# Kernel optimization log

Measured on AMD Instinct MI355X. Metric: run time of the kernel, lower is better.

Reference implementation:

```python
import jax, jax.numpy as jnp
import numpy as np

N_HEAD = 16
MASK_SCALE = 10000.0  # matches torch buffer construction


def setup_inputs() -> dict:
    key = jax.random.key(0)
    k1, k2 = jax.random.split(key)
    B, T, C = 2, 2048, 1024
    x = jax.random.normal(k1, (B, T, C), dtype=jnp.float32)
    # packed q,k projection: nn.Linear(C, 2C, bias=False) -> weight [2C, C]
    W_attn = jax.random.normal(k2, (2 * C, C), dtype=jnp.float32) * 0.02
    alpha = jnp.array(1.0, dtype=jnp.float32)
    beta = jnp.array(0.1, dtype=jnp.float32)
    gamma = jnp.array(0.1, dtype=jnp.float32)
    return {"x": x, "W_attn": W_attn, "alpha": alpha, "beta": beta, "gamma": gamma}


def _shaped_attention(x, W_attn, alpha, beta, gamma):
    B, T, C = x.shape
    H = N_HEAD
    hd = C // H
    # packed projection then split into q, k (use_v=False -> v comes from x)
    qk = jnp.einsum('btc,oc->bto', x, W_attn)  # [B,T,2C]
    q, k = jnp.split(qk, 2, axis=-1)
    q = q.reshape(B, T, H, hd).transpose(0, 2, 1, 3)  # [B,H,T,hd]
    k = k.reshape(B, T, H, hd).transpose(0, 2, 1, 3)
    v = x.reshape(B, T, H, hd).transpose(0, 2, 1, 3)

    scores = jnp.einsum('bhqd,bhkd->bhqk', q, k) * (hd ** -0.5)
    tril = jnp.tril(jnp.ones((T, T), dtype=bool))
    scores = jnp.where(tril, scores, -jnp.inf)
    att = jax.nn.softmax(scores, axis=-1)  # [B,H,T,T]

    # fixed structured masks, built exactly as the torch buffers
    Id = jax.nn.softmax(jnp.eye(T, dtype=jnp.float32) * MASK_SCALE, axis=-1)
    MC = jax.nn.softmax(tril.astype(jnp.float32) * MASK_SCALE, axis=-1)

    shaped = beta * att + alpha * Id[None, None] - gamma * MC[None, None]
    y = jnp.einsum('bhqk,bhkd->bhqd', shaped, v)
    return y.transpose(0, 2, 1, 3).reshape(B, T, C)  # c_proj is Identity


def reference(x, W_attn, alpha, beta, gamma):
    return _shaped_attention(x, W_attn, alpha, beta, gamma)
```

## Files before the change

### kernel.cpp

```cpp
#include <hip/hip_runtime.h>
#include <hip/hip_bf16.h>

typedef __attribute__((ext_vector_type(8))) short bf16x8;
typedef __attribute__((ext_vector_type(4))) float f32x4;
typedef unsigned short u16;

#define B_  2
#define T_  2048
#define C_  1024
#define H_  16
#define HD_ 64

static __device__ __forceinline__ u16 f2bf(float f) {
  unsigned u = __float_as_uint(f);
  u += 0x7fffu + ((u >> 16) & 1u);
  return (u16)(u >> 16);
}

#define NW4 524288
__global__ __launch_bounds__(256) void prep(
    const float* __restrict__ X, const float* __restrict__ W,
    u16* __restrict__ Xb, u16* __restrict__ Wb,
    u16* __restrict__ Vf, float* __restrict__ SubP64)
{
  __shared__ u16 tr[64][65];
  __shared__ float cs[4][64];
  const int blk = blockIdx.x;
  const int tid = threadIdx.x;

  if (blk < 1024) {
    const int kt = blk & 31, bh = blk >> 5;
    const int b = bh >> 4, h = bh & 15;
    const int w = tid >> 6, lane = tid & 63;
    {
      const int row = tid >> 2;
      const int c0  = (tid & 3) * 16;
      const float* xp = X + ((size_t)b * T_ + kt * 64 + row) * C_ + h * 64 + c0;
      float vals[16];
#pragma unroll
      for (int q = 0; q < 4; ++q) {
        float4 v = *(const float4*)(xp + q * 4);
        vals[q * 4 + 0] = v.x; vals[q * 4 + 1] = v.y;
        vals[q * 4 + 2] = v.z; vals[q * 4 + 3] = v.w;
      }
      u16 xb[16];
#pragma unroll
      for (int i = 0; i < 16; ++i) xb[i] = f2bf(vals[i]);
      u16* xq = Xb + ((size_t)(b * T_ + kt * 64 + row)) * C_ + h * 64 + c0;
      *(bf16x8*)xq       = *(const bf16x8*)&xb[0];
      *(bf16x8*)(xq + 8) = *(const bf16x8*)&xb[8];
#pragma unroll
      for (int i = 0; i < 16; ++i) tr[row][c0 + i] = xb[i];
#pragma unroll
      for (int m = 4; m <= 32; m <<= 1)
#pragma unroll
        for (int i = 0; i < 16; ++i) vals[i] += __shfl_xor(vals[i], m);
      if (lane < 4) {
        float* dst = &cs[w][lane * 16];
#pragma unroll
        for (int q = 0; q < 4; ++q) {
          f32x4 s4 = { vals[q * 4 + 0], vals[q * 4 + 1], vals[q * 4 + 2], vals[q * 4 + 3] };
          *(f32x4*)&dst[q * 4] = s4;
        }
      }
    }
    __syncthreads();
    {
      const int quad = (lane >> 4), l16 = lane & 15;
      u16* outb = Vf + ((size_t)bh * 32 + kt) * 4096;
#pragma unroll
      for (int c = 0; c < 2; ++c) {
        u16 tmp[8];
#pragma unroll
        for (int j = 0; j < 8; ++j) tmp[j] = tr[c * 32 + quad * 8 + j][w * 16 + l16];
        *(bf16x8*)&outb[((w * 2 + c) * 64 + lane) * 8] = *(const bf16x8*)tmp;
      }
    }
    if (tid < 64)
      SubP64[(size_t)bh * 2048 + kt * 64 + tid] =
          cs[0][tid] + cs[1][tid] + cs[2][tid] + cs[3][tid];
  } else {
    int i = (blk - 1024) * 256 + tid;
    float4 v = ((const float4*)W)[i];
    ushort4 u = { f2bf(v.x), f2bf(v.y), f2bf(v.z), f2bf(v.w) };
    ((ushort4*)Wb)[i] = u;
  }
}

__global__ __launch_bounds__(256) void gemm_qk(
    const u16* __restrict__ Xb, const u16* __restrict__ Wb,
    u16* __restrict__ Qo, u16* __restrict__ Kf)
{
  __shared__ __align__(16) u16 As[2][128 * 64];
  __shared__ __align__(16) u16 Bs[2][128 * 64];

  const int tid  = threadIdx.x;
  const int w    = tid >> 6;
  const int lane = tid & 63;
  const int quad = lane >> 4;
  const int l16  = lane & 15;
  const int m0 = blockIdx.y * 128;
  const int n0 = blockIdx.x * 128;

  const int grow = w * 8 + ((lane >> 3) & 7);
  const int gcol = (lane & 7) * 8;

  f32x4 zero = {0.f, 0.f, 0.f, 0.f};
  f32x4 acc[4][4];
#pragma unroll
  for (int i = 0; i < 4; ++i)
#pragma unroll
    for (int j = 0; j < 4; ++j) acc[i][j] = zero;

  const int wr = (w >> 1) * 64, wc = (w & 1) * 64;

  const u16* gax = Xb + (size_t)(m0 + grow) * C_ + gcol;
  const u16* gbx = Wb + (size_t)(n0 + grow) * C_ + gcol;

#define GISSUE(K, BUF)                                                      \
  {                                                                         \
    _Pragma("unroll") for (int r = 0; r < 4; ++r) {                         \
      __builtin_amdgcn_global_load_lds(                                     \
          (const __attribute__((address_space(1))) void*)(gax + (size_t)r * 32 * C_ + (K)), \
          (__attribute__((address_space(3))) void*)&As[BUF][(w * 8 + r * 32) * 64], \
          16, 0, 0);                                                        \
      __builtin_amdgcn_global_load_lds(                                     \
          (const __attribute__((address_space(1))) void*)(gbx + (size_t)r * 32 * C_ + (K)), \
          (__attribute__((address_space(3))) void*)&Bs[BUF][(w * 8 + r * 32) * 64], \
          16, 0, 0);                                                        \
    }                                                                       \
  }

  GISSUE(0, 0);
#pragma unroll 2
  for (int it = 0; it < 16; ++it) {
    const int cur = it & 1;
    __syncthreads();
    if (it < 15) GISSUE((it + 1) * 64, cur ^ 1);
#pragma unroll
    for (int c = 0; c < 2; ++c) {
      bf16x8 af[4], bf[4];
#pragma unroll
      for (int i = 0; i < 4; ++i)
        af[i] = *(const bf16x8*)&As[cur][(wr + i * 16 + l16) * 64 + c * 32 + quad * 8];
#pragma unroll
      for (int j = 0; j < 4; ++j)
        bf[j] = *(const bf16x8*)&Bs[cur][(wc + j * 16 + l16) * 64 + c * 32 + quad * 8];
#pragma unroll
      for (int i = 0; i < 4; ++i)
#pragma unroll
        for (int j = 0; j < 4; ++j)
          acc[i][j] = __builtin_amdgcn_mfma_f32_16x16x32_bf16(af[i], bf[j], acc[i][j], 0, 0, 0);
    }
  }
#undef GISSUE

#pragma unroll
  for (int i = 0; i < 4; ++i) {
    const int t_base = m0 + wr + i * 16;
    const int bidx = t_base >> 11;
    const int kt   = (t_base & 2047) >> 6;
    const int trow = (t_base & 2047) + quad * 4;
#pragma unroll
    for (int j = 0; j < 4; ++j) {
      const int n = n0 + wc + j * 16 + l16;
      if (n < C_) {
        const int hq = n >> 6, d = n & 63;
        u16* qp = Qo + (((size_t)bidx * H_ + hq) * T_ + trow) * HD_ + d;
#pragma unroll
        for (int r = 0; r < 4; ++r) qp[(size_t)r * HD_] = f2bf(0.125f * acc[i][j][r]);
      } else {
        const int nh = n - C_;
        const int hh = nh >> 6, d = nh & 63;
        u16* kp = Kf + (((((size_t)(bidx * H_ + hh) * 32 + kt) * 4 + i) * 2 + (d >> 5)) * 64
                        + ((d >> 3) & 3) * 16 + quad * 4) * 8 + (d & 7);
#pragma unroll
        for (int r = 0; r < 4; ++r) kp[(size_t)r * 8] = f2bf(acc[i][j][r]);
      }
    }
  }
}

__device__ __forceinline__ void load_kv(
    bf16x8 (&kf)[2][4], bf16x8 (&vf)[2][4],
    const u16* __restrict__ kbase, const u16* __restrict__ vbase, int lane)
{
#pragma unroll
  for (int c = 0; c < 2; ++c)
#pragma unroll
    for (int nb = 0; nb < 4; ++nb) {
      kf[c][nb] = *(const bf16x8*)&kbase[((nb * 2 + c) * 64 + lane) * 8];
      vf[c][nb] = *(const bf16x8*)&vbase[((nb * 2 + c) * 64 + lane) * 8];
    }
}

__device__ __forceinline__ void tile_compute(
    const bf16x8 (&qfrag)[2], const bf16x8 (&kf)[2][4], const bf16x8 (&vf)[2][4],
    f32x4 (&acc)[4], f32x4& accl, float (*pb)[68],
    int quad, int l16, int myrow, bool diag, bf16x8 onesf)
{
  f32x4 zero = {0.f, 0.f, 0.f, 0.f};
  f32x4 sfr[4] = {zero, zero, zero, zero};
#pragma unroll
  for (int cc = 0; cc < 2; ++cc)
#pragma unroll
    for (int nb = 0; nb < 4; ++nb)
      sfr[nb] = __builtin_amdgcn_mfma_f32_16x16x32_bf16(qfrag[cc], kf[cc][nb], sfr[nb], 0, 0, 0);

#pragma unroll
  for (int nb = 0; nb < 4; ++nb)
#pragma unroll
    for (int r = 0; r < 4; ++r) {
      float p = __expf(sfr[nb][r]);
      if (diag && (nb * 16 + l16 > myrow + r)) p = 0.f;
      pb[quad * 4 + r][nb * 16 + l16] = p;
    }

#pragma unroll
  for (int cc = 0; cc < 2; ++cc) {
    f32x4 plo = *(const f32x4*)&pb[l16][cc * 32 + quad * 8];
    f32x4 phi = *(const f32x4*)&pb[l16][cc * 32 + quad * 8 + 4];
    union { unsigned u[4]; bf16x8 v; } pk;
    __hip_bfloat162 hh;
    hh = __float22bfloat162_rn(make_float2(plo[0], plo[1])); pk.u[0] = *(unsigned*)&hh;
    hh = __float22bfloat162_rn(make_float2(plo[2], plo[3])); pk.u[1] = *(unsigned*)&hh;
    hh = __float22bfloat162_rn(make_float2(phi[0], phi[1])); pk.u[2] = *(unsigned*)&hh;
    hh = __float22bfloat162_rn(make_float2(phi[2], phi[3])); pk.u[3] = *(unsigned*)&hh;
    accl = __builtin_amdgcn_mfma_f32_16x16x32_bf16(pk.v, onesf, accl, 0, 0, 0);
#pragma unroll
    for (int nb = 0; nb < 4; ++nb)
      acc[nb] = __builtin_amdgcn_mfma_f32_16x16x32_bf16(pk.v, vf[cc][nb], acc[nb], 0, 0, 0);
  }
}

__global__ __launch_bounds__(256) void attn_kernel(
    const u16* __restrict__ Q, const u16* __restrict__ Kf, const u16* __restrict__ Vf,
    const float* __restrict__ SubP64, const float* __restrict__ X, float* __restrict__ out,
    const float* __restrict__ alphap, const float* __restrict__ betap,
    const float* __restrict__ gammap)
{
  __shared__ __align__(16) char smem[19456];

  const int tid  = threadIdx.x;
  const int w    = tid >> 6;
  const int lane = tid & 63;
  const int quad = lane >> 4;
  const int l16  = lane & 15;
  const int qt = 31 - blockIdx.y;
  const int bh = blockIdx.x;
  const int b = bh >> 4, h = bh & 15;

  const u16* kfb = Kf + (size_t)bh * T_ * HD_;
  const u16* vfb = Vf + (size_t)bh * T_ * HD_;

  bf16x8 qfrag[2];
  {
    const u16* qp = Q + ((size_t)bh * T_ + qt * 64 + w * 16 + l16) * HD_ + quad * 8;
    qfrag[0] = *(const bf16x8*)qp;
    qfrag[1] = *(const bf16x8*)(qp + 32);
  }

  bf16x8 onesf;
#pragma unroll
  for (int j = 0; j < 8; ++j) onesf[j] = (short)0x3F80;

  f32x4 zero = {0.f, 0.f, 0.f, 0.f};
  f32x4 acc[4] = {zero, zero, zero, zero};
  f32x4 accl = zero;
  const int myrow = w * 16 + quad * 4;
  float (*pb)[68] = (float(*)[68])((float*)smem + (size_t)w * 16 * 68);

  bf16x8 kA[2][4], vA[2][4], kB[2][4], vB[2][4];
  load_kv(kA, vA, kfb, vfb, lane);
  int kt = 0;
  for (;;) {
    int ktn = (kt + 1 < qt) ? kt + 1 : qt;
    load_kv(kB, vB, kfb + (size_t)ktn * 4096, vfb + (size_t)ktn * 4096, lane);
    tile_compute(qfrag, kA, vA, acc, accl, pb, quad, l16, myrow, kt == qt, onesf);
    if (kt + 1 > qt) break;
    int ktn2 = (kt + 2 < qt) ? kt + 2 : qt;
    load_kv(kA, vA, kfb + (size_t)ktn2 * 4096, vfb + (size_t)ktn2 * 4096, lane);
    tile_compute(qfrag, kB, vB, acc, accl, pb, quad, l16, myrow, kt + 1 == qt, onesf);
    kt += 2;
    if (kt > qt) break;
  }

  __syncthreads();
  float* Xt = (float*)smem;
  float* G  = (float*)(smem + 17408);
  float* GP = (float*)(smem + 18432);

  {
    const int row = tid >> 2, c0 = (tid & 3) * 16;
    const float* xp = X + ((size_t)b * T_ + qt * 64 + row) * C_ + h * 64 + c0;
#pragma unroll
    for (int q = 0; q < 4; ++q) {
      float4 v = *(const float4*)(xp + q * 4);
      Xt[row * 68 + c0 + q * 4 + 0] = v.x;
      Xt[row * 68 + c0 + q * 4 + 1] = v.y;
      Xt[row * 68 + c0 + q * 4 + 2] = v.z;
      Xt[row * 68 + c0 + q * 4 + 3] = v.w;
    }
  }
  {
    float p = 0.f;
    for (int i = w; i < qt; i += 4)
      p += SubP64[(size_t)bh * 2048 + i * 64 + lane];
    GP[w * 64 + lane] = p;
  }
  __syncthreads();
  {
    float g = 0.f;
#pragma unroll
    for (int i = 0; i < 16; ++i) g += Xt[(w * 16 + i) * 68 + lane];
    G[w * 64 + lane] = g;
  }
  __syncthreads();
  {
    const float alpha = *alphap, gamma = *gammap;
    float run = GP[lane] + GP[64 + lane] + GP[128 + lane] + GP[192 + lane];
    for (int g = 0; g < w; ++g) run += G[g * 64 + lane];
    const int tbase = qt * 64 + w * 16;
#pragma unroll
    for (int i = 0; i < 16; ++i) {
      float v = Xt[(w * 16 + i) * 68 + lane];
      run += v;
      Xt[(w * 16 + i) * 68 + lane] =
          alpha * v - gamma * run * __builtin_amdgcn_rcpf((float)(tbase + i + 1));
    }
  }
  __syncthreads();

  const float beta = *betap;
  float rl[4];
#pragma unroll
  for (int r = 0; r < 4; ++r) rl[r] = beta * __builtin_amdgcn_rcpf(accl[r]);
#pragma unroll
  for (int nb = 0; nb < 4; ++nb) {
#pragma unroll
    for (int r = 0; r < 4; ++r) {
      int t = qt * 64 + myrow + r;
      int d = nb * 16 + l16;
      out[((size_t)b * T_ + t) * C_ + h * 64 + d] =
          Xt[(myrow + r) * 68 + d] + rl[r] * acc[nb][r];
    }
  }
}

extern "C" void kernel_launch(void* const* d_in, const int* in_sizes, int n_in,
                              void* d_out, int out_size, void* d_ws, size_t ws_size,
                              hipStream_t stream) {
  const float* x      = (const float*)d_in[0];
  const float* W_attn = (const float*)d_in[1];
  const float* alphap = (const float*)d_in[2];
  const float* betap  = (const float*)d_in[3];
  const float* gammap = (const float*)d_in[4];
  float* out = (float*)d_out;

  char* ws = (char*)d_ws;
  u16*   Qb     = (u16*)(ws);
  u16*   Kfb    = (u16*)(ws + (8ull  << 20));
  u16*   Vfb    = (u16*)(ws + (16ull << 20));
  float* SubP64 = (float*)(ws + (24ull << 20));
  u16*   Xb     = (u16*)(ws + (25ull << 20));
  u16*   Wb     = (u16*)(ws + (33ull << 20));

  prep<<<3072, 256, 0, stream>>>(x, W_attn, Xb, Wb, Vfb, SubP64);
  gemm_qk<<<dim3(16, 32), 256, 0, stream>>>(Xb, Wb, Qb, Kfb);
  attn_kernel<<<dim3(32, 32), 256, 0, stream>>>(Qb, Kfb, Vfb, SubP64, x, out,
                                                alphap, betap, gammap);
}
```

Before: 151.1 us.

## Split attention key loop across two wave groups per block and combine partials

Result: slower. 310.7 us (+105.7%).

```diff
diff --git a/kernel.cpp b/kernel.cpp
--- a/kernel.cpp
+++ b/kernel.cpp
@@ -66,6 +66,7 @@
     }
     __syncthreads();
     {
+      const int w = tid >> 6, lane = tid & 63;
       const int quad = (lane >> 4), l16 = lane & 15;
       u16* outb = Vf + ((size_t)bh * 32 + kt) * 4096;
 #pragma unroll
@@ -233,16 +234,18 @@
   }
 }
 
-__global__ __launch_bounds__(256) void attn_kernel(
+__global__ __launch_bounds__(512, 6) void attn_kernel(
     const u16* __restrict__ Q, const u16* __restrict__ Kf, const u16* __restrict__ Vf,
     const float* __restrict__ SubP64, const float* __restrict__ X, float* __restrict__ out,
     const float* __restrict__ alphap, const float* __restrict__ betap,
     const float* __restrict__ gammap)
 {
-  __shared__ __align__(16) char smem[19456];
+  __shared__ __align__(16) char smem[34816];
 
   const int tid  = threadIdx.x;
   const int w    = tid >> 6;
+  const int wq   = w & 3;
+  const int half = w >> 2;
   const int lane = tid & 63;
   const int quad = lane >> 4;
   const int l16  = lane & 15;
@@ -255,7 +258,7 @@
 
   bf16x8 qfrag[2];
   {
-    const u16* qp = Q + ((size_t)bh * T_ + qt * 64 + w * 16 + l16) * HD_ + quad * 8;
+    const u16* qp = Q + ((size_t)bh * T_ + qt * 64 + wq * 16 + l16) * HD_ + quad * 8;
     qfrag[0] = *(const bf16x8*)qp;
     qfrag[1] = *(const bf16x8*)(qp + 32);
   }
@@ -267,34 +270,57 @@
   f32x4 zero = {0.f, 0.f, 0.f, 0.f};
   f32x4 acc[4] = {zero, zero, zero, zero};
   f32x4 accl = zero;
-  const int myrow = w * 16 + quad * 4;
+  const int myrow = wq * 16 + quad * 4;
   float (*pb)[68] = (float(*)[68])((float*)smem + (size_t)w * 16 * 68);
 
-  bf16x8 kA[2][4], vA[2][4], kB[2][4], vB[2][4];
-  load_kv(kA, vA, kfb, vfb, lane);
-  int kt = 0;
-  for (;;) {
-    int ktn = (kt + 1 < qt) ? kt + 1 : qt;
-    load_kv(kB, vB, kfb + (size_t)ktn * 4096, vfb + (size_t)ktn * 4096, lane);
-    tile_compute(qfrag, kA, vA, acc, accl, pb, quad, l16, myrow, kt == qt, onesf);
-    if (kt + 1 > qt) break;
-    int ktn2 = (kt + 2 < qt) ? kt + 2 : qt;
-    load_kv(kA, vA, kfb + (size_t)ktn2 * 4096, vfb + (size_t)ktn2 * 4096, lane);
-    tile_compute(qfrag, kB, vB, acc, accl, pb, quad, l16, myrow, kt + 1 == qt, onesf);
-    kt += 2;
-    if (kt > qt) break;
+  if (half <= qt) {
+    bf16x8 kA[2][4], vA[2][4], kB[2][4], vB[2][4];
+    int kt = half;
+    load_kv(kA, vA, kfb + (size_t)kt * 4096, vfb + (size_t)kt * 4096, lane);
+    for (;;) {
+      int ktn = (kt + 2 <= qt) ? kt + 2 : kt;
+      load_kv(kB, vB, kfb + (size_t)ktn * 4096, vfb + (size_t)ktn * 4096, lane);
+      tile_compute(qfrag, kA, vA, acc, accl, pb, quad, l16, myrow, kt == qt, onesf);
+      if (kt + 2 > qt) break;
+      int ktn2 = (kt + 4 <= qt) ? kt + 4 : kt + 2;
+      load_kv(kA, vA, kfb + (size_t)ktn2 * 4096, vfb + (size_t)ktn2 * 4096, lane);
+      tile_compute(qfrag, kB, vB, acc, accl, pb, quad, l16, myrow, kt + 2 == qt, onesf);
+      kt += 4;
+      if (kt > qt) break;
+    }
   }
 
   __syncthreads();
+  {
+    float* comb = (float*)smem;
+    if (half == 1) {
+      float* dst = comb + ((size_t)(wq * 64 + lane)) * 20;
+#pragma unroll
+      for (int nb = 0; nb < 4; ++nb) *(f32x4*)&dst[nb * 4] = acc[nb];
+      *(f32x4*)&dst[16] = accl;
+    }
+    __syncthreads();
+    if (half == 0) {
+      const float* src = comb + ((size_t)(wq * 64 + lane)) * 20;
+#pragma unroll
+      for (int nb = 0; nb < 4; ++nb) {
+        f32x4 t = *(const f32x4*)&src[nb * 4];
+        acc[nb] += t;
+      }
+      accl += *(const f32x4*)&src[16];
+    }
+  }
+  __syncthreads();
+
   float* Xt = (float*)smem;
   float* G  = (float*)(smem + 17408);
-  float* GP = (float*)(smem + 18432);
-
-  {
-    const int row = tid >> 2, c0 = (tid & 3) * 16;
+  float* GP = (float*)(smem + 19456);
+
+  {
+    const int row = tid >> 3, c0 = (tid & 7) * 8;
     const float* xp = X + ((size_t)b * T_ + qt * 64 + row) * C_ + h * 64 + c0;
 #pragma unroll
-    for (int q = 0; q < 4; ++q) {
+    for (int q = 0; q < 2; ++q) {
       float4 v = *(const float4*)(xp + q * 4);
       Xt[row * 68 + c0 + q * 4 + 0] = v.x;
       Xt[row * 68 + c0 + q * 4 + 1] = v.y;
@@ -304,7 +330,7 @@
   }
   {
     float p = 0.f;
-    for (int i = w; i < qt; i += 4)
+    for (int i = w; i < qt; i += 8)
       p += SubP64[(size_t)bh * 2048 + i * 64 + lane];
     GP[w * 64 + lane] = p;
   }
@@ -312,37 +338,41 @@
   {
     float g = 0.f;
 #pragma unroll
-    for (int i = 0; i < 16; ++i) g += Xt[(w * 16 + i) * 68 + lane];
+    for (int i = 0; i < 8; ++i) g += Xt[(w * 8 + i) * 68 + lane];
     G[w * 64 + lane] = g;
   }
   __syncthreads();
   {
     const float alpha = *alphap, gamma = *gammap;
-    float run = GP[lane] + GP[64 + lane] + GP[128 + lane] + GP[192 + lane];
+    float run = 0.f;
+#pragma unroll
+    for (int k = 0; k < 8; ++k) run += GP[k * 64 + lane];
     for (int g = 0; g < w; ++g) run += G[g * 64 + lane];
-    const int tbase = qt * 64 + w * 16;
-#pragma unroll
-    for (int i = 0; i < 16; ++i) {
-      float v = Xt[(w * 16 + i) * 68 + lane];
+    const int tbase = qt * 64 + w * 8;
+#pragma unroll
+    for (int i = 0; i < 8; ++i) {
+      float v = Xt[(w * 8 + i) * 68 + lane];
       run += v;
-      Xt[(w * 16 + i) * 68 + lane] =
+      Xt[(w * 8 + i) * 68 + lane] =
           alpha * v - gamma * run * __builtin_amdgcn_rcpf((float)(tbase + i + 1));
     }
   }
   __syncthreads();
 
-  const float beta = *betap;
-  float rl[4];
-#pragma unroll
-  for (int r = 0; r < 4; ++r) rl[r] = beta * __builtin_amdgcn_rcpf(accl[r]);
-#pragma unroll
-  for (int nb = 0; nb < 4; ++nb) {
-#pragma unroll
-    for (int r = 0; r < 4; ++r) {
-      int t = qt * 64 + myrow + r;
-      int d = nb * 16 + l16;
-      out[((size_t)b * T_ + t) * C_ + h * 64 + d] =
-          Xt[(myrow + r) * 68 + d] + rl[r] * acc[nb][r];
+  if (half == 0) {
+    const float beta = *betap;
+    float rl[4];
+#pragma unroll
+    for (int r = 0; r < 4; ++r) rl[r] = beta * __builtin_amdgcn_rcpf(accl[r]);
+#pragma unroll
+    for (int nb = 0; nb < 4; ++nb) {
+#pragma unroll
+      for (int r = 0; r < 4; ++r) {
+        int t = qt * 64 + myrow + r;
+        int d = nb * 16 + l16;
+        out[((size_t)b * T_ + t) * C_ + h * 64 + d] =
+            Xt[(myrow + r) * 68 + d] + rl[r] * acc[nb][r];
+      }
     }
   }
 }
@@ -367,6 +397,6 @@
 
   prep<<<3072, 256, 0, stream>>>(x, W_attn, Xb, Wb, Vfb, SubP64);
   gemm_qk<<<dim3(16, 32), 256, 0, stream>>>(Xb, Wb, Qb, Kfb);
-  attn_kernel<<<dim3(32, 32), 256, 0, stream>>>(Qb, Kfb, Vfb, SubP64, x, out,
+  attn_kernel<<<dim3(32, 32), 512, 0, stream>>>(Qb, Kfb, Vfb, SubP64, x, out,
                                                 alphap, betap, gammap);
 }
```

## Share LDS-staged K/V tiles across 128-row attention blocks with async double buffering

Applied to the files above, without the earlier changes.

Result: no change. 150.4 us (-0.5%).

```diff
diff --git a/kernel.cpp b/kernel.cpp
--- a/kernel.cpp
+++ b/kernel.cpp
@@ -66,6 +66,7 @@
     }
     __syncthreads();
     {
+      const int w = tid >> 6, lane = tid & 63;
       const int quad = (lane >> 4), l16 = lane & 15;
       u16* outb = Vf + ((size_t)bh * 32 + kt) * 4096;
 #pragma unroll
@@ -181,81 +182,36 @@
   }
 }
 
-__device__ __forceinline__ void load_kv(
-    bf16x8 (&kf)[2][4], bf16x8 (&vf)[2][4],
-    const u16* __restrict__ kbase, const u16* __restrict__ vbase, int lane)
-{
-#pragma unroll
-  for (int c = 0; c < 2; ++c)
-#pragma unroll
-    for (int nb = 0; nb < 4; ++nb) {
-      kf[c][nb] = *(const bf16x8*)&kbase[((nb * 2 + c) * 64 + lane) * 8];
-      vf[c][nb] = *(const bf16x8*)&vbase[((nb * 2 + c) * 64 + lane) * 8];
-    }
-}
-
-__device__ __forceinline__ void tile_compute(
-    const bf16x8 (&qfrag)[2], const bf16x8 (&kf)[2][4], const bf16x8 (&vf)[2][4],
-    f32x4 (&acc)[4], f32x4& accl, float (*pb)[68],
-    int quad, int l16, int myrow, bool diag, bf16x8 onesf)
-{
-  f32x4 zero = {0.f, 0.f, 0.f, 0.f};
-  f32x4 sfr[4] = {zero, zero, zero, zero};
-#pragma unroll
-  for (int cc = 0; cc < 2; ++cc)
-#pragma unroll
-    for (int nb = 0; nb < 4; ++nb)
-      sfr[nb] = __builtin_amdgcn_mfma_f32_16x16x32_bf16(qfrag[cc], kf[cc][nb], sfr[nb], 0, 0, 0);
-
-#pragma unroll
-  for (int nb = 0; nb < 4; ++nb)
-#pragma unroll
-    for (int r = 0; r < 4; ++r) {
-      float p = __expf(sfr[nb][r]);
-      if (diag && (nb * 16 + l16 > myrow + r)) p = 0.f;
-      pb[quad * 4 + r][nb * 16 + l16] = p;
-    }
-
-#pragma unroll
-  for (int cc = 0; cc < 2; ++cc) {
-    f32x4 plo = *(const f32x4*)&pb[l16][cc * 32 + quad * 8];
-    f32x4 phi = *(const f32x4*)&pb[l16][cc * 32 + quad * 8 + 4];
-    union { unsigned u[4]; bf16x8 v; } pk;
-    __hip_bfloat162 hh;
-    hh = __float22bfloat162_rn(make_float2(plo[0], plo[1])); pk.u[0] = *(unsigned*)&hh;
-    hh = __float22bfloat162_rn(make_float2(plo[2], plo[3])); pk.u[1] = *(unsigned*)&hh;
-    hh = __float22bfloat162_rn(make_float2(phi[0], phi[1])); pk.u[2] = *(unsigned*)&hh;
-    hh = __float22bfloat162_rn(make_float2(phi[2], phi[3])); pk.u[3] = *(unsigned*)&hh;
-    accl = __builtin_amdgcn_mfma_f32_16x16x32_bf16(pk.v, onesf, accl, 0, 0, 0);
-#pragma unroll
-    for (int nb = 0; nb < 4; ++nb)
-      acc[nb] = __builtin_amdgcn_mfma_f32_16x16x32_bf16(pk.v, vf[cc][nb], acc[nb], 0, 0, 0);
-  }
-}
-
-__global__ __launch_bounds__(256) void attn_kernel(
+__global__ __launch_bounds__(512) void attn_kernel(
     const u16* __restrict__ Q, const u16* __restrict__ Kf, const u16* __restrict__ Vf,
     const float* __restrict__ SubP64, const float* __restrict__ X, float* __restrict__ out,
     const float* __restrict__ alphap, const float* __restrict__ betap,
     const float* __restrict__ gammap)
 {
-  __shared__ __align__(16) char smem[19456];
+  __shared__ __align__(16) char smem[51200];
+  u16 (*Ks)[4096] = (u16(*)[4096])(smem);
+  u16 (*Vs)[4096] = (u16(*)[4096])(smem + 16384);
 
   const int tid  = threadIdx.x;
   const int w    = tid >> 6;
   const int lane = tid & 63;
   const int quad = lane >> 4;
   const int l16  = lane & 15;
-  const int qt = 31 - blockIdx.y;
+  const int jq = 15 - blockIdx.y;
   const int bh = blockIdx.x;
   const int b = bh >> 4, h = bh & 15;
 
+  const int qt_w  = 2 * jq + (w >> 2);
+  const int qtmax = 2 * jq + 1;
+  const int mt    = (w & 3) * 16 + quad * 4;
+
   const u16* kfb = Kf + (size_t)bh * T_ * HD_;
   const u16* vfb = Vf + (size_t)bh * T_ * HD_;
+  u16* pb = (u16*)(smem + 32768) + (size_t)w * 1152;
 
   bf16x8 qfrag[2];
   {
-    const u16* qp = Q + ((size_t)bh * T_ + qt * 64 + w * 16 + l16) * HD_ + quad * 8;
+    const u16* qp = Q + ((size_t)bh * T_ + jq * 128 + w * 16 + l16) * HD_ + quad * 8;
     qfrag[0] = *(const bf16x8*)qp;
     qfrag[1] = *(const bf16x8*)(qp + 32);
   }
@@ -267,32 +223,71 @@
   f32x4 zero = {0.f, 0.f, 0.f, 0.f};
   f32x4 acc[4] = {zero, zero, zero, zero};
   f32x4 accl = zero;
-  const int myrow = w * 16 + quad * 4;
-  float (*pb)[68] = (float(*)[68])((float*)smem + (size_t)w * 16 * 68);
-
-  bf16x8 kA[2][4], vA[2][4], kB[2][4], vB[2][4];
-  load_kv(kA, vA, kfb, vfb, lane);
-  int kt = 0;
-  for (;;) {
-    int ktn = (kt + 1 < qt) ? kt + 1 : qt;
-    load_kv(kB, vB, kfb + (size_t)ktn * 4096, vfb + (size_t)ktn * 4096, lane);
-    tile_compute(qfrag, kA, vA, acc, accl, pb, quad, l16, myrow, kt == qt, onesf);
-    if (kt + 1 > qt) break;
-    int ktn2 = (kt + 2 < qt) ? kt + 2 : qt;
-    load_kv(kA, vA, kfb + (size_t)ktn2 * 4096, vfb + (size_t)ktn2 * 4096, lane);
-    tile_compute(qfrag, kB, vB, acc, accl, pb, quad, l16, myrow, kt + 1 == qt, onesf);
-    kt += 2;
-    if (kt > qt) break;
-  }
+
+#define STAGE(KT, BUF)                                                        \
+  {                                                                           \
+    const u16* sb = (w < 4) ? kfb : vfb;                                      \
+    u16* db = (w < 4) ? &Ks[BUF][0] : &Vs[BUF][0];                            \
+    const int ch = (w & 3) * 2;                                               \
+    _Pragma("unroll") for (int ci = 0; ci < 2; ++ci) {                        \
+      __builtin_amdgcn_global_load_lds(                                       \
+          (const __attribute__((address_space(1))) void*)(                    \
+              sb + (size_t)(KT) * 4096 + (ch + ci) * 512 + lane * 8),         \
+          (__attribute__((address_space(3))) void*)(db + (ch + ci) * 512),    \
+          16, 0, 0);                                                          \
+    }                                                                         \
+  }
+
+  STAGE(0, 0);
+  for (int kt = 0; kt <= qtmax; ++kt) {
+    const int cur = kt & 1;
+    __syncthreads();
+    if (kt < qtmax) STAGE(kt + 1, cur ^ 1);
+    if (kt <= qt_w) {
+      const u16* Ksb = Ks[cur];
+      const u16* Vsb = Vs[cur];
+      const bool diag = (kt == qt_w);
+
+      f32x4 sfr[4] = {zero, zero, zero, zero};
+#pragma unroll
+      for (int cc = 0; cc < 2; ++cc)
+#pragma unroll
+        for (int nb = 0; nb < 4; ++nb) {
+          bf16x8 kf = *(const bf16x8*)&Ksb[((nb * 2 + cc) * 64 + lane) * 8];
+          sfr[nb] = __builtin_amdgcn_mfma_f32_16x16x32_bf16(qfrag[cc], kf, sfr[nb], 0, 0, 0);
+        }
+
+#pragma unroll
+      for (int nb = 0; nb < 4; ++nb)
+#pragma unroll
+        for (int r = 0; r < 4; ++r) {
+          float p = __expf(sfr[nb][r]);
+          if (diag && (nb * 16 + l16 > mt + r)) p = 0.f;
+          pb[(quad * 4 + r) * 72 + nb * 16 + l16] = f2bf(p);
+        }
+
+#pragma unroll
+      for (int cc = 0; cc < 2; ++cc) {
+        bf16x8 pk = *(const bf16x8*)&pb[l16 * 72 + cc * 32 + quad * 8];
+        accl = __builtin_amdgcn_mfma_f32_16x16x32_bf16(pk, onesf, accl, 0, 0, 0);
+#pragma unroll
+        for (int nb = 0; nb < 4; ++nb) {
+          bf16x8 vf = *(const bf16x8*)&Vsb[((nb * 2 + cc) * 64 + lane) * 8];
+          acc[nb] = __builtin_amdgcn_mfma_f32_16x16x32_bf16(pk, vf, acc[nb], 0, 0, 0);
+        }
+      }
+    }
+  }
+#undef STAGE
 
   __syncthreads();
   float* Xt = (float*)smem;
-  float* G  = (float*)(smem + 17408);
-  float* GP = (float*)(smem + 18432);
+  float* G  = (float*)(smem + 34816);
+  float* GP = (float*)(smem + 36864);
 
   {
     const int row = tid >> 2, c0 = (tid & 3) * 16;
-    const float* xp = X + ((size_t)b * T_ + qt * 64 + row) * C_ + h * 64 + c0;
+    const float* xp = X + ((size_t)b * T_ + jq * 128 + row) * C_ + h * 64 + c0;
 #pragma unroll
     for (int q = 0; q < 4; ++q) {
       float4 v = *(const float4*)(xp + q * 4);
@@ -304,7 +299,7 @@
   }
   {
     float p = 0.f;
-    for (int i = w; i < qt; i += 4)
+    for (int i = w; i < 2 * jq; i += 8)
       p += SubP64[(size_t)bh * 2048 + i * 64 + lane];
     GP[w * 64 + lane] = p;
   }
@@ -318,9 +313,11 @@
   __syncthreads();
   {
     const float alpha = *alphap, gamma = *gammap;
-    float run = GP[lane] + GP[64 + lane] + GP[128 + lane] + GP[192 + lane];
+    float run = 0.f;
+#pragma unroll
+    for (int k = 0; k < 8; ++k) run += GP[k * 64 + lane];
     for (int g = 0; g < w; ++g) run += G[g * 64 + lane];
-    const int tbase = qt * 64 + w * 16;
+    const int tbase = jq * 128 + w * 16;
 #pragma unroll
     for (int i = 0; i < 16; ++i) {
       float v = Xt[(w * 16 + i) * 68 + lane];
@@ -331,18 +328,21 @@
   }
   __syncthreads();
 
-  const float beta = *betap;
-  float rl[4];
-#pragma unroll
-  for (int r = 0; r < 4; ++r) rl[r] = beta * __builtin_amdgcn_rcpf(accl[r]);
-#pragma unroll
-  for (int nb = 0; nb < 4; ++nb) {
-#pragma unroll
-    for (int r = 0; r < 4; ++r) {
-      int t = qt * 64 + myrow + r;
-      int d = nb * 16 + l16;
-      out[((size_t)b * T_ + t) * C_ + h * 64 + d] =
-          Xt[(myrow + r) * 68 + d] + rl[r] * acc[nb][r];
+  {
+    const float beta = *betap;
+    float rl[4];
+#pragma unroll
+    for (int r = 0; r < 4; ++r) rl[r] = beta * __builtin_amdgcn_rcpf(accl[r]);
+    const int myrow = w * 16 + quad * 4;
+#pragma unroll
+    for (int nb = 0; nb < 4; ++nb) {
+#pragma unroll
+      for (int r = 0; r < 4; ++r) {
+        int t = jq * 128 + myrow + r;
+        int d = nb * 16 + l16;
+        out[((size_t)b * T_ + t) * C_ + h * 64 + d] =
+            Xt[(myrow + r) * 68 + d] + rl[r] * acc[nb][r];
+      }
     }
   }
 }
@@ -367,6 +367,6 @@
 
   prep<<<3072, 256, 0, stream>>>(x, W_attn, Xb, Wb, Vfb, SubP64);
   gemm_qk<<<dim3(16, 32), 256, 0, stream>>>(Xb, Wb, Qb, Kfb);
-  attn_kernel<<<dim3(32, 32), 256, 0, stream>>>(Qb, Kfb, Vfb, SubP64, x, out,
+  attn_kernel<<<dim3(32, 16), 512, 0, stream>>>(Qb, Kfb, Vfb, SubP64, x, out,
                                                 alphap, betap, gammap);
 }
```
